# Optimization experiments

Measured on AMD Instinct MI355X. Metric: run time of the kernel, lower is better.

Reference implementation:

```python
import jax, jax.numpy as jnp
import numpy as np

B, SEG, P, H, NH = 8, 16, 256, 1024, 16
DH = H // NH
T = P + 1                 # tokens per segment (segment lord + segment_size)
L = 1 + SEG * T           # 4113
LN_EPS = 1e-12


def setup_inputs() -> dict:
    key = jax.random.key(0)
    ks = jax.random.split(key, 9)
    s = 0.02
    return {
        "hidden_states": jax.random.normal(ks[0], (B, L, H), jnp.float32),
        "Blord_w": jax.random.normal(ks[1], (H, H), jnp.float32) * s,
        "Blord_b": jnp.zeros((H,), jnp.float32),
        "seg_qw": jax.random.normal(ks[2], (SEG, H, H), jnp.float32) * s,
        "seg_kw": jax.random.normal(ks[3], (SEG, H, H), jnp.float32) * s,
        "seg_vw": jax.random.normal(ks[4], (SEG, H, H), jnp.float32) * s,
        "lord_qw": jax.random.normal(ks[5], (H, H), jnp.float32) * s,
        "lord_kw": jax.random.normal(ks[6], (H, H), jnp.float32) * s,
        "lord_vw": jax.random.normal(ks[7], (H, H), jnp.float32) * s,
        "out_w": jax.random.normal(ks[8], (H, H), jnp.float32) * s,
        "out_b": jnp.zeros((H,), jnp.float32),
        "ln_w": jnp.ones((H,), jnp.float32),
        "ln_b": jnp.zeros((H,), jnp.float32),
    }


def reference(hidden_states, Blord_w, Blord_b, seg_qw, seg_kw, seg_vw,
              lord_qw, lord_kw, lord_vw, out_w, out_b, ln_w, ln_b):
    scale = 1.0 / np.sqrt(DH).astype(np.float32)

    # global lord projection of token 0 (torch Linear: x @ W.T + b)
    Blord = hidden_states[:, 0] @ Blord_w.T + Blord_b              # [B,H]

    # per-segment local full attention (each segment has its own QKV weights)
    seg_x = hidden_states[:, 1:].reshape(B, SEG, T, H)             # [B,S,T,H]
    q = jnp.einsum('bsti,soi->bsto', seg_x, seg_qw).reshape(B, SEG, T, NH, DH)
    k = jnp.einsum('bsti,soi->bsto', seg_x, seg_kw).reshape(B, SEG, T, NH, DH)
    v = jnp.einsum('bsti,soi->bsto', seg_x, seg_vw).reshape(B, SEG, T, NH, DH)
    scores = jnp.einsum('bsqhd,bskhd->bshqk', q, k) * scale        # [B,S,NH,T,T]
    probs = jax.nn.softmax(scores, axis=-1)
    seg_out = jnp.einsum('bshqk,bskhd->bsqhd', probs, v).reshape(B, SEG, T, H)

    # global attention over lord tokens: [Blord, seg_out[:, :, 0]]
    lords_in = jnp.concatenate([Blord[:, None, :], seg_out[:, :, 0, :]], axis=1)  # [B,S+1,H]
    lq = (lords_in @ lord_qw.T).reshape(B, SEG + 1, NH, DH)
    lk = (lords_in @ lord_kw.T).reshape(B, SEG + 1, NH, DH)
    lv = (lords_in @ lord_vw.T).reshape(B, SEG + 1, NH, DH)
    lscores = jnp.einsum('bqhd,bkhd->bhqk', lq, lk) * scale        # [B,NH,S+1,S+1]
    lprobs = jax.nn.softmax(lscores, axis=-1)
    lords = jnp.einsum('bhqk,bkhd->bqhd', lprobs, lv).reshape(B, SEG + 1, H)

    # reassemble: global lord, then per segment (updated lord token, local tokens)
    seg_out = seg_out.at[:, :, 0, :].set(lords[:, 1:])
    self_outputs = jnp.concatenate(
        [lords[:, :1], seg_out.reshape(B, SEG * T, H)], axis=1)    # [B,L,H]

    # output dense + residual + LayerNorm
    h = self_outputs @ out_w.T + out_b + hidden_states
    mu = h.mean(axis=-1, keepdims=True)
    var = h.var(axis=-1, keepdims=True)
    attention_output = (h - mu) / jnp.sqrt(var + LN_EPS) * ln_w + ln_b
    return attention_output, self_outputs
```

## Files before the change

### kernel.cpp

```cpp
#include <hip/hip_runtime.h>
#include <hip/hip_bf16.h>

typedef long long ll;
typedef __attribute__((ext_vector_type(8))) short bf16x8;
typedef __attribute__((ext_vector_type(4))) float fx4;

#define B_ 8
#define SEG_ 16
#define T_ 257
#define H_ 1024
#define NH_ 16
#define L_ 4113
#define SCALE 0.125f

__device__ __forceinline__ unsigned short f2bfu(float x) {
  __hip_bfloat16 h = __float2bfloat16(x);
  return *(unsigned short*)&h;
}

__device__ __forceinline__ void gl_lds16(const void* g, void* l) {
  __builtin_amdgcn_global_load_lds((const __attribute__((address_space(1))) void*)g,
                                   (__attribute__((address_space(3))) void*)l, 16, 0, 0);
}

#define NU_HID 4211712
#define NU_W   2097152
#define NU_OW  131072
__global__ __launch_bounds__(256) void f2bf_all(
    const float* __restrict__ hid, __hip_bfloat16* __restrict__ hbf,
    const float* __restrict__ wq, const float* __restrict__ wk, const float* __restrict__ wv,
    __hip_bfloat16* __restrict__ w3,
    const float* __restrict__ ow, __hip_bfloat16* __restrict__ owb)
{
  const int NTOT = NU_HID + 3 * NU_W + NU_OW;
  for (int i = blockIdx.x * 256 + threadIdx.x; i < NTOT; i += gridDim.x * 256) {
    const float* src;
    __hip_bfloat16* dst;
    if (i < NU_HID) {
      src = hid + (ll)i * 8;
      dst = hbf + (ll)i * 8;
    } else if (i < NU_HID + 3 * NU_W) {
      int j = i - NU_HID;
      int which = j >> 21;
      int off = j & (NU_W - 1);
      const float* ws = (which == 0) ? wq : (which == 1) ? wk : wv;
      src = ws + (ll)off * 8;
      dst = w3 + (ll)j * 8;
    } else {
      int k = i - NU_HID - 3 * NU_W;
      src = ow + (ll)k * 8;
      dst = owb + (ll)k * 8;
    }
    float4 a = ((const float4*)src)[0];
    float4 b = ((const float4*)src)[1];
    union { bf16x8 v; unsigned short u[8]; } o;
    o.u[0] = f2bfu(a.x); o.u[1] = f2bfu(a.y); o.u[2] = f2bfu(a.z); o.u[3] = f2bfu(a.w);
    o.u[4] = f2bfu(b.x); o.u[5] = f2bfu(b.y); o.u[6] = f2bfu(b.z); o.u[7] = f2bfu(b.w);
    *(bf16x8*)dst = o.v;
  }
}

__global__ __launch_bounds__(256) void gemm_qkv(
    const __hip_bfloat16* __restrict__ A,
    const __hip_bfloat16* __restrict__ Wall,
    __hip_bfloat16* __restrict__ Cq,
    __hip_bfloat16* __restrict__ Ck,
    __hip_bfloat16* __restrict__ Cv)
{
  const int nwg = 24 * 17 * 16;
  const int orig = blockIdx.x + 24 * (blockIdx.y + 17 * blockIdx.z);
  const int swz = (orig & 7) * (nwg >> 3) + (orig >> 3);
  const int bx = swz % 24;
  const int t2 = swz / 24;
  const int by = t2 % 17;
  const int bz = t2 / 17;
  const int which = bx >> 3;
  const int n0 = (bx & 7) * 128;
  const int m0 = by * 128;
  const int M = B_ * T_;

  const __hip_bfloat16* W = Wall + ((ll)which * SEG_ + bz) * ((ll)H_ * H_);
  __hip_bfloat16* C = (which == 0) ? Cq : (which == 1) ? Ck : Cv;

  __shared__ __hip_bfloat16 At[2][128 * 32];
  __shared__ __hip_bfloat16 Bt[2][128 * 32];

  const int tid = threadIdx.x;
  const int lane = tid & 63;
  const int wid = tid >> 6;
  const int wm = (wid >> 1) * 64;
  const int wn = (wid & 1) * 64;

  const int r0 = tid >> 2;
  const int kc = (tid & 3) * 8;
  const int am0 = min(m0 + r0, M - 1);
  const int am1 = min(m0 + 64 + r0, M - 1);
  const ll segoff = (ll)bz * ((ll)T_ * H_);
  const ll aoff0 = (ll)(am0 / T_) * ((ll)L_ * H_) + segoff + (ll)(am0 % T_) * H_;
  const ll aoff1 = (ll)(am1 / T_) * ((ll)L_ * H_) + segoff + (ll)(am1 % T_) * H_;
  const ll boff0 = (ll)(n0 + r0) * H_;
  const ll boff1 = (ll)(n0 + 64 + r0) * H_;
  const int stA0 = r0 * 32 + kc;

  fx4 acc[4][4];
#pragma unroll
  for (int i = 0; i < 4; ++i)
#pragma unroll
    for (int j = 0; j < 4; ++j) acc[i][j] = fx4{0.f, 0.f, 0.f, 0.f};

  const int fragA = (wm + (lane & 15)) * 32 + ((lane >> 4) << 3);
  const int fragB = (wn + (lane & 15)) * 32 + ((lane >> 4) << 3);

  gl_lds16(A + aoff0 + kc, (void*)(&At[0][0] + stA0));
  gl_lds16(A + aoff1 + kc, (void*)(&At[0][0] + 2048 + stA0));
  gl_lds16(W + boff0 + kc, (void*)(&Bt[0][0] + stA0));
  gl_lds16(W + boff1 + kc, (void*)(&Bt[0][0] + 2048 + stA0));
  __syncthreads();

  int cur = 0;
  for (int k0 = 0; k0 < 1024; k0 += 32) {
    if (k0 + 32 < 1024) {
      const int kn = k0 + 32;
      const int nxt = cur ^ 1;
      gl_lds16(A + aoff0 + kn + kc, (void*)(&At[nxt][0] + stA0));
      gl_lds16(A + aoff1 + kn + kc, (void*)(&At[nxt][0] + 2048 + stA0));
      gl_lds16(W + boff0 + kn + kc, (void*)(&Bt[nxt][0] + stA0));
      gl_lds16(W + boff1 + kn + kc, (void*)(&Bt[nxt][0] + 2048 + stA0));
    }

    const __hip_bfloat16* ap = &At[cur][0] + fragA;
    const __hip_bfloat16* bp = &Bt[cur][0] + fragB;
    bf16x8 af[4], bfr[4];
#pragma unroll
    for (int f = 0; f < 4; ++f) {
      af[f]  = *(const bf16x8*)(ap + f * 16 * 32);
      bfr[f] = *(const bf16x8*)(bp + f * 16 * 32);
    }
#pragma unroll
    for (int mf = 0; mf < 4; ++mf)
#pragma unroll
      for (int nf = 0; nf < 4; ++nf)
        acc[mf][nf] = __builtin_amdgcn_mfma_f32_16x16x32_bf16(af[mf], bfr[nf], acc[mf][nf], 0, 0, 0);

    __syncthreads();
    cur ^= 1;
  }

  const int cn = n0 + wn + (lane & 15);
#pragma unroll
  for (int mf = 0; mf < 4; ++mf) {
    int mloc = m0 + wm + mf * 16 + ((lane >> 4) << 2);
#pragma unroll
    for (int r = 0; r < 4; ++r) {
      int m = mloc + r;
      if (m >= M) continue;
      ll co = ((ll)(m / T_) * SEG_ + bz) * ((ll)T_ * H_) + (ll)(m % T_) * H_;
#pragma unroll
      for (int nf = 0; nf < 4; ++nf)
        C[co + cn + nf * 16] = __float2bfloat16(acc[mf][nf][r]);
    }
  }
}

__global__ __launch_bounds__(256) void gemm_out(
    const __hip_bfloat16* __restrict__ A,
    const __hip_bfloat16* __restrict__ W,
    const float* __restrict__ bias,
    float* __restrict__ C,
    const float* __restrict__ res)
{
  const int nwg = 8 * 258;
  const int orig = blockIdx.x + 8 * blockIdx.y;
  const int swz = (orig & 7) * (nwg >> 3) + (orig >> 3);
  const int bx = swz % 8;
  const int by = swz / 8;
  const int M = B_ * L_;
  const int m0 = by * 128;
  const int n0 = bx * 128;

  __shared__ __hip_bfloat16 At[2][128 * 32];
  __shared__ __hip_bfloat16 Bt[2][128 * 32];

  const int tid = threadIdx.x;
  const int lane = tid & 63;
  const int wid = tid >> 6;
  const int wm = (wid >> 1) * 64;
  const int wn = (wid & 1) * 64;

  const int r0 = tid >> 2;
  const int kc = (tid & 3) * 8;
  const ll aoff0 = (ll)min(m0 + r0, M - 1) * H_;
  const ll aoff1 = (ll)min(m0 + 64 + r0, M - 1) * H_;
  const ll boff0 = (ll)(n0 + r0) * H_;
  const ll boff1 = (ll)(n0 + 64 + r0) * H_;
  const int stA0 = r0 * 32 + kc;

  fx4 acc[4][4];
#pragma unroll
  for (int i = 0; i < 4; ++i)
#pragma unroll
    for (int j = 0; j < 4; ++j) acc[i][j] = fx4{0.f, 0.f, 0.f, 0.f};

  const int fragA = (wm + (lane & 15)) * 32 + ((lane >> 4) << 3);
  const int fragB = (wn + (lane & 15)) * 32 + ((lane >> 4) << 3);

  gl_lds16(A + aoff0 + kc, (void*)(&At[0][0] + stA0));
  gl_lds16(A + aoff1 + kc, (void*)(&At[0][0] + 2048 + stA0));
  gl_lds16(W + boff0 + kc, (void*)(&Bt[0][0] + stA0));
  gl_lds16(W + boff1 + kc, (void*)(&Bt[0][0] + 2048 + stA0));
  __syncthreads();

  int cur = 0;
  for (int k0 = 0; k0 < 1024; k0 += 32) {
    if (k0 + 32 < 1024) {
      const int kn = k0 + 32;
      const int nxt = cur ^ 1;
      gl_lds16(A + aoff0 + kn + kc, (void*)(&At[nxt][0] + stA0));
      gl_lds16(A + aoff1 + kn + kc, (void*)(&At[nxt][0] + 2048 + stA0));
      gl_lds16(W + boff0 + kn + kc, (void*)(&Bt[nxt][0] + stA0));
      gl_lds16(W + boff1 + kn + kc, (void*)(&Bt[nxt][0] + 2048 + stA0));
    }

    const __hip_bfloat16* ap = &At[cur][0] + fragA;
    const __hip_bfloat16* bp = &Bt[cur][0] + fragB;
    bf16x8 af[4], bfr[4];
#pragma unroll
    for (int f = 0; f < 4; ++f) {
      af[f]  = *(const bf16x8*)(ap + f * 16 * 32);
      bfr[f] = *(const bf16x8*)(bp + f * 16 * 32);
    }
#pragma unroll
    for (int mf = 0; mf < 4; ++mf)
#pragma unroll
      for (int nf = 0; nf < 4; ++nf)
        acc[mf][nf] = __builtin_amdgcn_mfma_f32_16x16x32_bf16(af[mf], bfr[nf], acc[mf][nf], 0, 0, 0);

    __syncthreads();
    cur ^= 1;
  }

  const int cn = n0 + wn + (lane & 15);
#pragma unroll
  for (int mf = 0; mf < 4; ++mf) {
    int mloc = m0 + wm + mf * 16 + ((lane >> 4) << 2);
#pragma unroll
    for (int r = 0; r < 4; ++r) {
      int m = mloc + r;
      if (m >= M) continue;
#pragma unroll
      for (int nf = 0; nf < 4; ++nf) {
        int n = cn + nf * 16;
        C[(ll)m * H_ + n] = acc[mf][nf][r] + bias[n] + res[(ll)m * H_ + n];
      }
    }
  }
}

__global__ __launch_bounds__(256) void seg_attn_mfma(
    const __hip_bfloat16* __restrict__ Qb,
    const __hip_bfloat16* __restrict__ Kb,
    const __hip_bfloat16* __restrict__ Vb,
    float* __restrict__ so, __hip_bfloat16* __restrict__ sob)
{
  __shared__ __align__(16) char smem[8192 + 9216 + 4 * 4096];
  char* KsB = smem;
  char* VTB = smem + 8192;
  const int tid = threadIdx.x, lane = tid & 63, wid = tid >> 6;
  char* PB = smem + 8192 + 9216 + wid * 4096;

  const int h = blockIdx.y, bs = blockIdx.z;
  const int b = bs >> 4, s = bs & 15;
  const int q0 = blockIdx.x * 128 + wid * 32;
  const bool qvalid = (q0 <= 256);
  const ll base = (ll)bs * (T_ * H_) + h * 64;

  bf16x8 qf[2][2];
#pragma unroll
  for (int mf = 0; mf < 2; ++mf) {
    int qr = q0 + mf * 16 + (lane & 15); if (qr > 256) qr = 256;
#pragma unroll
    for (int ks = 0; ks < 2; ++ks)
      qf[mf][ks] = *(const bf16x8*)(Qb + base + (ll)qr * H_ + ks * 32 + ((lane >> 4) << 3));
  }

  float l_[2][4];
  fx4 of[2][4];
#pragma unroll
  for (int mf = 0; mf < 2; ++mf) {
#pragma unroll
    for (int r = 0; r < 4; ++r) l_[mf][r] = 0.f;
#pragma unroll
    for (int df = 0; df < 4; ++df) of[mf][df] = fx4{0.f, 0.f, 0.f, 0.f};
  }

  const int krow = tid >> 3;
  const int kc8 = tid & 7;
  const int kkp = tid & 31;
  const int vd0 = (tid >> 5) * 8;

  for (int t = 0; t < 5; ++t) {
    const int k0 = t * 64;
    __syncthreads();
    {
      int row = krow;
      int kr = k0 + row; if (kr > 256) kr = 256;
      gl_lds16(Kb + base + (ll)kr * H_ + ((kc8 ^ (row & 7)) << 3), KsB + tid * 16);
      row = krow + 32;
      kr = k0 + row; if (kr > 256) kr = 256;
      gl_lds16(Kb + base + (ll)kr * H_ + ((kc8 ^ (row & 7)) << 3), KsB + 4096 + tid * 16);
    }
    {
      int kk = kkp * 2;
      int kr0 = k0 + kk;     if (kr0 > 256) kr0 = 256;
      int kr1 = k0 + kk + 1; if (kr1 > 256) kr1 = 256;
      bf16x8 v0 = *(const bf16x8*)(Vb + base + (ll)kr0 * H_ + vd0);
      bf16x8 v1 = *(const bf16x8*)(Vb + base + (ll)kr1 * H_ + vd0);
      unsigned int* vtu = (unsigned int*)VTB;
#pragma unroll
      for (int j = 0; j < 8; ++j)
        vtu[(vd0 + j) * 36 + kkp] =
            (unsigned int)(unsigned short)v0[j] | ((unsigned int)(unsigned short)v1[j] << 16);
    }
    __syncthreads();

    if (qvalid) {
      fx4 sa[2][4];
#pragma unroll
      for (int mf = 0; mf < 2; ++mf)
#pragma unroll
        for (int nf = 0; nf < 4; ++nf) sa[mf][nf] = fx4{0.f, 0.f, 0.f, 0.f};
#pragma unroll
      for (int nf = 0; nf < 4; ++nf) {
        int key = nf * 16 + (lane & 15);
#pragma unroll
        for (int ks = 0; ks < 2; ++ks) {
          int c16 = ks * 4 + (lane >> 4);
          bf16x8 kf = *(const bf16x8*)(KsB + key * 128 + ((c16 ^ (key & 7)) << 4));
          sa[0][nf] = __builtin_amdgcn_mfma_f32_16x16x32_bf16(qf[0][ks], kf, sa[0][nf], 0, 0, 0);
          sa[1][nf] = __builtin_amdgcn_mfma_f32_16x16x32_bf16(qf[1][ks], kf, sa[1][nf], 0, 0, 0);
        }
      }
#pragma unroll
      for (int nf = 0; nf < 4; ++nf) {
        bool bad = (k0 + nf * 16 + (lane & 15)) > 256;
#pragma unroll
        for (int mf = 0; mf < 2; ++mf) {
#pragma unroll
          for (int r = 0; r < 4; ++r) {
            float p = bad ? 0.f : __expf(sa[mf][nf][r] * SCALE);
            sa[mf][nf][r] = p;
            l_[mf][r] += p;
          }
        }
      }
#pragma unroll
      for (int mf = 0; mf < 2; ++mf)
#pragma unroll
        for (int nf = 0; nf < 4; ++nf)
#pragma unroll
          for (int rp = 0; rp < 2; ++rp) {
            float v0 = sa[mf][nf][rp];
            float v2 = sa[mf][nf][rp + 2];
            float o0 = __shfl_xor(v0, 1);
            float o2 = __shfl_xor(v2, 1);
            const bool odd = (lane & 1);
            float lo = odd ? o2 : v0;
            float hi = odd ? v2 : o0;
            unsigned int pk = (unsigned int)f2bfu(lo) | ((unsigned int)f2bfu(hi) << 16);
            int row = mf * 16 + ((lane >> 4) << 2) + (odd ? rp + 2 : rp);
            int col2 = nf * 16 + (lane & 14);
            *(unsigned int*)(PB + row * 128 + ((col2 * 2) ^ ((row & 7) << 4))) = pk;
          }
#pragma unroll
      for (int kks = 0; kks < 2; ++kks) {
        bf16x8 pa[2];
#pragma unroll
        for (int mf = 0; mf < 2; ++mf) {
          int prow = mf * 16 + (lane & 15);
          int c16 = kks * 4 + (lane >> 4);
          pa[mf] = *(const bf16x8*)(PB + prow * 128 + ((c16 ^ (prow & 7)) << 4));
        }
#pragma unroll
        for (int df = 0; df < 4; ++df) {
          bf16x8 vf = *(const bf16x8*)(VTB + (df * 16 + (lane & 15)) * 144 + kks * 64 + ((lane >> 4) << 4));
          of[0][df] = __builtin_amdgcn_mfma_f32_16x16x32_bf16(pa[0], vf, of[0][df], 0, 0, 0);
          of[1][df] = __builtin_amdgcn_mfma_f32_16x16x32_bf16(pa[1], vf, of[1][df], 0, 0, 0);
        }
      }
    }
  }

  if (qvalid) {
#pragma unroll
    for (int mf = 0; mf < 2; ++mf)
#pragma unroll
      for (int r = 0; r < 4; ++r) {
        float rs = l_[mf][r];
        rs += __shfl_xor(rs, 1);
        rs += __shfl_xor(rs, 2);
        rs += __shfl_xor(rs, 4);
        rs += __shfl_xor(rs, 8);
        l_[mf][r] = rs;
      }
#pragma unroll
    for (int mf = 0; mf < 2; ++mf)
#pragma unroll
      for (int r = 0; r < 4; ++r) {
        int q = q0 + mf * 16 + ((lane >> 4) << 2) + r;
        if (q > 256) continue;
        float inv = 1.f / l_[mf][r];
        ll rowoff = ((ll)b * L_ + 1 + (ll)s * T_ + q) * H_ + h * 64;
#pragma unroll
        for (int df = 0; df < 4; ++df) {
          int d = df * 16 + (lane & 15);
          float v = of[mf][df][r] * inv;
          so[rowoff + d] = v;
          sob[rowoff + d] = __float2bfloat16(v);
        }
      }
  }
}

__global__ __launch_bounds__(256) void gemm_bt(
    const float* __restrict__ X, ll xbs,
    const float* __restrict__ W,
    const float* __restrict__ bias,
    float* __restrict__ C, ll cbs,
    int M, int K)
{
  const int tid = threadIdx.x;
  const int n0 = blockIdx.x * 64;

  __shared__ float Xt[16][68];
  __shared__ float Wt[16][68];

  const int lr = tid >> 2;
  const int lc = (tid & 3) << 2;
  const int mload = min(lr, M - 1);
  const ll xoff = (ll)mload * xbs;
  const ll woff = (ll)(n0 + lr) * K;

  const int tr = tid >> 4;
  const int tc = tid & 15;

  float acc[4][4];
#pragma unroll
  for (int i = 0; i < 4; ++i)
#pragma unroll
    for (int j = 0; j < 4; ++j) acc[i][j] = 0.f;

  for (int k0 = 0; k0 < K; k0 += 16) {
    float4 xv = *(const float4*)(X + xoff + k0 + lc);
    float4 wv = *(const float4*)(W + woff + k0 + lc);
    __syncthreads();
    Xt[lc + 0][lr] = xv.x; Xt[lc + 1][lr] = xv.y; Xt[lc + 2][lr] = xv.z; Xt[lc + 3][lr] = xv.w;
    Wt[lc + 0][lr] = wv.x; Wt[lc + 1][lr] = wv.y; Wt[lc + 2][lr] = wv.z; Wt[lc + 3][lr] = wv.w;
    __syncthreads();
#pragma unroll
    for (int kk = 0; kk < 16; ++kk) {
      float4 xa = *(const float4*)&Xt[kk][tr << 2];
      float4 wb = *(const float4*)&Wt[kk][tc << 2];
      float xa_[4] = {xa.x, xa.y, xa.z, xa.w};
      float wb_[4] = {wb.x, wb.y, wb.z, wb.w};
#pragma unroll
      for (int i = 0; i < 4; ++i)
#pragma unroll
        for (int j = 0; j < 4; ++j)
          acc[i][j] = fmaf(xa_[i], wb_[j], acc[i][j]);
    }
  }

#pragma unroll
  for (int i = 0; i < 4; ++i) {
    int m = (tr << 2) + i;
    if (m >= M) continue;
#pragma unroll
    for (int j = 0; j < 4; ++j) {
      int n = n0 + (tc << 2) + j;
      C[(ll)m * cbs + n] = acc[i][j] + (bias ? bias[n] : 0.f);
    }
  }
}

__global__ __launch_bounds__(256) void lord_proj(
    const float* __restrict__ X,
    const float* __restrict__ Wq, const float* __restrict__ Wk, const float* __restrict__ Wv,
    float* __restrict__ Cq, float* __restrict__ Ck, float* __restrict__ Cv)
{
  const float* W = (blockIdx.z == 0) ? Wq : (blockIdx.z == 1) ? Wk : Wv;
  float* C = (blockIdx.z == 0) ? Cq : (blockIdx.z == 1) ? Ck : Cv;
  const int M = 136, K = 1024;

  const int tid = threadIdx.x;
  const int m0 = blockIdx.y * 64;
  const int n0 = blockIdx.x * 64;

  __shared__ float Xt[16][68];
  __shared__ float Wt[16][68];

  const int lr = tid >> 2;
  const int lc = (tid & 3) << 2;
  const int mload = min(m0 + lr, M - 1);
  const ll xoff = (ll)mload * K;
  const ll woff = (ll)(n0 + lr) * K;

  const int tr = tid >> 4;
  const int tc = tid & 15;

  float acc[4][4];
#pragma unroll
  for (int i = 0; i < 4; ++i)
#pragma unroll
    for (int j = 0; j < 4; ++j) acc[i][j] = 0.f;

  for (int k0 = 0; k0 < K; k0 += 16) {
    float4 xv = *(const float4*)(X + xoff + k0 + lc);
    float4 wv = *(const float4*)(W + woff + k0 + lc);
    __syncthreads();
    Xt[lc + 0][lr] = xv.x; Xt[lc + 1][lr] = xv.y; Xt[lc + 2][lr] = xv.z; Xt[lc + 3][lr] = xv.w;
    Wt[lc + 0][lr] = wv.x; Wt[lc + 1][lr] = wv.y; Wt[lc + 2][lr] = wv.z; Wt[lc + 3][lr] = wv.w;
    __syncthreads();
#pragma unroll
    for (int kk = 0; kk < 16; ++kk) {
      float4 xa = *(const float4*)&Xt[kk][tr << 2];
      float4 wb = *(const float4*)&Wt[kk][tc << 2];
      float xa_[4] = {xa.x, xa.y, xa.z, xa.w};
      float wb_[4] = {wb.x, wb.y, wb.z, wb.w};
#pragma unroll
      for (int i = 0; i < 4; ++i)
#pragma unroll
        for (int j = 0; j < 4; ++j)
          acc[i][j] = fmaf(xa_[i], wb_[j], acc[i][j]);
    }
  }

#pragma unroll
  for (int i = 0; i < 4; ++i) {
    int m = m0 + (tr << 2) + i;
    if (m >= M) continue;
#pragma unroll
    for (int j = 0; j < 4; ++j)
      C[(ll)m * 1024 + n0 + (tc << 2) + j] = acc[i][j];
  }
}

__global__ __launch_bounds__(256) void copy_lords_in(
    const float* __restrict__ so, float* __restrict__ lin)
{
  int b = blockIdx.x / SEG_, s = blockIdx.x % SEG_;
  int i = threadIdx.x * 4;
  *(float4*)(lin + ((ll)(b * 17 + 1 + s)) * H_ + i) =
      *(const float4*)(so + ((ll)b * L_ + 1 + (ll)s * T_) * H_ + i);
}

__global__ __launch_bounds__(256) void lord_attn2(
    const float* __restrict__ lq, const float* __restrict__ lk,
    const float* __restrict__ lv, float* __restrict__ so,
    __hip_bfloat16* __restrict__ sob)
{
  const int b = blockIdx.x, h = blockIdx.y;
  const int tid = threadIdx.x, lane = tid & 63, wid = tid >> 6;
  __shared__ float Qs[17][64], Ks[17][64], Vs[17][64];
  for (int t = tid; t < 17 * 64; t += 256) {
    int r = t >> 6, c = t & 63;
    ll g = ((ll)(b * 17 + r)) * H_ + h * 64 + c;
    Qs[r][c] = lq[g];
    Ks[r][c] = lk[g];
    Vs[r][c] = lv[g];
  }
  __syncthreads();
  for (int q = wid; q < 17; q += 4) {
    float qd = Qs[q][lane];
    float sc[17];
#pragma unroll
    for (int k = 0; k < 17; ++k) {
      float p = qd * Ks[k][lane];
      p += __shfl_xor(p, 1);  p += __shfl_xor(p, 2);  p += __shfl_xor(p, 4);
      p += __shfl_xor(p, 8);  p += __shfl_xor(p, 16); p += __shfl_xor(p, 32);
      sc[k] = p * SCALE;
    }
    float mx = sc[0];
#pragma unroll
    for (int k = 1; k < 17; ++k) mx = fmaxf(mx, sc[k]);
    float l = 0.f;
#pragma unroll
    for (int k = 0; k < 17; ++k) { sc[k] = __expf(sc[k] - mx); l += sc[k]; }
    float invl = 1.f / l;
    float o = 0.f;
#pragma unroll
    for (int k = 0; k < 17; ++k) o = fmaf(sc[k], Vs[k][lane], o);
    o *= invl;
    ll row = (q == 0) ? (ll)b * L_ : ((ll)b * L_ + 1 + (ll)(q - 1) * T_);
    so[row * H_ + h * 64 + lane] = o;
    sob[row * H_ + h * 64 + lane] = __float2bfloat16(o);
  }
}

__global__ __launch_bounds__(256) void ln_inplace(
    float* __restrict__ hbuf, const float* __restrict__ w, const float* __restrict__ bgain)
{
  const ll row = blockIdx.x;
  const int tid = threadIdx.x;
  float4 x = *(float4*)(hbuf + row * H_ + tid * 4);
  float s = x.x + x.y + x.z + x.w;
  float s2 = x.x * x.x + x.y * x.y + x.z * x.z + x.w * x.w;
#pragma unroll
  for (int off = 32; off >= 1; off >>= 1) {
    s  += __shfl_down(s, off, 64);
    s2 += __shfl_down(s2, off, 64);
  }
  __shared__ float red[2][4];
  int wid = tid >> 6;
  if ((tid & 63) == 0) { red[0][wid] = s; red[1][wid] = s2; }
  __syncthreads();
  s  = red[0][0] + red[0][1] + red[0][2] + red[0][3];
  s2 = red[1][0] + red[1][1] + red[1][2] + red[1][3];
  const float mean = s * (1.f / H_);
  float var = s2 * (1.f / H_) - mean * mean;
  var = fmaxf(var, 0.f);
  const float inv = rsqrtf(var + 1e-12f);
  float4 g = *(const float4*)(w + tid * 4);
  float4 bb = *(const float4*)(bgain + tid * 4);
  float4 y;
  y.x = (x.x - mean) * inv * g.x + bb.x;
  y.y = (x.y - mean) * inv * g.y + bb.y;
  y.z = (x.z - mean) * inv * g.z + bb.z;
  y.w = (x.w - mean) * inv * g.w + bb.w;
  *(float4*)(hbuf + row * H_ + tid * 4) = y;
}

extern "C" void kernel_launch(void* const* d_in, const int* in_sizes, int n_in,
                              void* d_out, int out_size, void* d_ws, size_t ws_size,
                              hipStream_t stream)
{
  const float* hidden  = (const float*)d_in[0];
  const float* Blord_w = (const float*)d_in[1];
  const float* Blord_b = (const float*)d_in[2];
  const float* seg_qw  = (const float*)d_in[3];
  const float* seg_kw  = (const float*)d_in[4];
  const float* seg_vw  = (const float*)d_in[5];
  const float* lord_qw = (const float*)d_in[6];
  const float* lord_kw = (const float*)d_in[7];
  const float* lord_vw = (const float*)d_in[8];
  const float* out_w   = (const float*)d_in[9];
  const float* out_b   = (const float*)d_in[10];
  const float* ln_w    = (const float*)d_in[11];
  const float* ln_b    = (const float*)d_in[12];

  float* attn_out = (float*)d_out;
  float* self_out = (float*)d_out + (ll)B_ * L_ * H_;

  const ll QKV = (ll)B_ * SEG_ * T_ * H_;
  const ll SHH = (ll)SEG_ * H_ * H_;
  __hip_bfloat16* qb = (__hip_bfloat16*)attn_out;
  __hip_bfloat16* kb = qb + QKV;
  __hip_bfloat16* hbf = (__hip_bfloat16*)self_out;
  __hip_bfloat16* vb = (__hip_bfloat16*)d_ws;
  __hip_bfloat16* wslot3 = vb + QKV;
  __hip_bfloat16* sob = wslot3;
  __hip_bfloat16* outw_bf = wslot3 + 3 * SHH;
  float* lords_in = (float*)(outw_bf + (ll)H_ * H_);
  float* lqw_ = lords_in + 136 * 1024;
  float* lkw_ = lqw_ + 136 * 1024;
  float* lvw_ = lkw_ + 136 * 1024;

  dim3 blk(256);

  f2bf_all<<<dim3(2048), blk, 0, stream>>>(
      hidden, hbf, seg_qw, seg_kw, seg_vw, wslot3, out_w, outw_bf);

  gemm_qkv<<<dim3(24, 17, 16), blk, 0, stream>>>(hbf + H_, wslot3, qb, kb, vb);

  gemm_bt<<<dim3(16), blk, 0, stream>>>(
      hidden, (ll)L_ * H_, Blord_w, Blord_b, lords_in, (ll)17 * H_, B_, H_);

  seg_attn_mfma<<<dim3(3, NH_, B_ * SEG_), blk, 0, stream>>>(qb, kb, vb, self_out, sob);

  copy_lords_in<<<dim3(B_ * SEG_), blk, 0, stream>>>(self_out, lords_in);

  lord_proj<<<dim3(16, 3, 3), blk, 0, stream>>>(
      lords_in, lord_qw, lord_kw, lord_vw, lqw_, lkw_, lvw_);

  lord_attn2<<<dim3(B_, NH_), blk, 0, stream>>>(lqw_, lkw_, lvw_, self_out, sob);

  gemm_out<<<dim3(8, 258), blk, 0, stream>>>(sob, outw_bf, out_b, attn_out, hidden);

  ln_inplace<<<dim3(B_ * L_), blk, 0, stream>>>(attn_out, ln_w, ln_b);
}
```

Measured before the change: 876.0 us.

## Triple-buffer GEMM K-loop with vmcnt waits and XOR-swizzled LDS tiles

Both the per-segment QKV GEMM and the output GEMM move from a double-buffered LDS pipeline to a three-stage one, prefetching two K-tiles ahead. They use explicit s_waitcnt vmcnt counts with raw barriers instead of __syncthreads. The global source column is XOR-swizzled per row, and the fragment read offset applies the matching swizzle, to cut LDS bank conflicts on the MFMA operand loads. This raises LDS use per block by half and relies on hand-counted outstanding loads being correct.

```diff
diff --git a/kernel.cpp b/kernel.cpp
--- a/kernel.cpp
+++ b/kernel.cpp
@@ -82,8 +82,8 @@
   const __hip_bfloat16* W = Wall + ((ll)which * SEG_ + bz) * ((ll)H_ * H_);
   __hip_bfloat16* C = (which == 0) ? Cq : (which == 1) ? Ck : Cv;
 
-  __shared__ __hip_bfloat16 At[2][128 * 32];
-  __shared__ __hip_bfloat16 Bt[2][128 * 32];
+  __shared__ __hip_bfloat16 At[3][128 * 32];
+  __shared__ __hip_bfloat16 Bt[3][128 * 32];
 
   const int tid = threadIdx.x;
   const int lane = tid & 63;
@@ -92,7 +92,9 @@
   const int wn = (wid & 1) * 64;
 
   const int r0 = tid >> 2;
-  const int kc = (tid & 3) * 8;
+  const int p = tid & 3;
+  const int kc  = p * 8;
+  const int kcs = (p ^ ((r0 >> 1) & 3)) * 8;
   const int am0 = min(m0 + r0, M - 1);
   const int am1 = min(m0 + 64 + r0, M - 1);
   const ll segoff = (ll)bz * ((ll)T_ * H_);
@@ -108,28 +110,31 @@
 #pragma unroll
     for (int j = 0; j < 4; ++j) acc[i][j] = fx4{0.f, 0.f, 0.f, 0.f};
 
-  const int fragA = (wm + (lane & 15)) * 32 + ((lane >> 4) << 3);
-  const int fragB = (wn + (lane & 15)) * 32 + ((lane >> 4) << 3);
-
-  gl_lds16(A + aoff0 + kc, (void*)(&At[0][0] + stA0));
-  gl_lds16(A + aoff1 + kc, (void*)(&At[0][0] + 2048 + stA0));
-  gl_lds16(W + boff0 + kc, (void*)(&Bt[0][0] + stA0));
-  gl_lds16(W + boff1 + kc, (void*)(&Bt[0][0] + 2048 + stA0));
-  __syncthreads();
-
-  int cur = 0;
-  for (int k0 = 0; k0 < 1024; k0 += 32) {
-    if (k0 + 32 < 1024) {
-      const int kn = k0 + 32;
-      const int nxt = cur ^ 1;
-      gl_lds16(A + aoff0 + kn + kc, (void*)(&At[nxt][0] + stA0));
-      gl_lds16(A + aoff1 + kn + kc, (void*)(&At[nxt][0] + 2048 + stA0));
-      gl_lds16(W + boff0 + kn + kc, (void*)(&Bt[nxt][0] + stA0));
-      gl_lds16(W + boff1 + kn + kc, (void*)(&Bt[nxt][0] + 2048 + stA0));
-    }
-
-    const __hip_bfloat16* ap = &At[cur][0] + fragA;
-    const __hip_bfloat16* bp = &Bt[cur][0] + fragB;
+  const int sw = ((lane & 15) >> 1) & 3;
+  const int fragA = (wm + (lane & 15)) * 32 + (((lane >> 4) ^ sw) << 3);
+  const int fragB = (wn + (lane & 15)) * 32 + (((lane >> 4) ^ sw) << 3);
+
+#define STAGE_QKV(buf, kt) do { const int kk = (kt) * 32; \
+    gl_lds16(A + aoff0 + kk + kcs, (void*)(&At[buf][0] + stA0)); \
+    gl_lds16(A + aoff1 + kk + kcs, (void*)(&At[buf][0] + 2048 + stA0)); \
+    gl_lds16(W + boff0 + kk + kcs, (void*)(&Bt[buf][0] + stA0)); \
+    gl_lds16(W + boff1 + kk + kcs, (void*)(&Bt[buf][0] + 2048 + stA0)); } while (0)
+
+  STAGE_QKV(0, 0);
+  STAGE_QKV(1, 1);
+  for (int t = 0; t < 32; ++t) {
+    __builtin_amdgcn_s_barrier();
+    asm volatile("" ::: "memory");
+    if (t + 2 < 32) { const int b3 = (t + 2) % 3; STAGE_QKV(b3, t + 2); }
+    if (t < 30)       asm volatile("s_waitcnt vmcnt(8)" ::: "memory");
+    else if (t == 30) asm volatile("s_waitcnt vmcnt(4)" ::: "memory");
+    else              asm volatile("s_waitcnt vmcnt(0)" ::: "memory");
+    __builtin_amdgcn_s_barrier();
+    asm volatile("" ::: "memory");
+
+    const int cb = t % 3;
+    const __hip_bfloat16* ap = &At[cb][0] + fragA;
+    const __hip_bfloat16* bp = &Bt[cb][0] + fragB;
     bf16x8 af[4], bfr[4];
 #pragma unroll
     for (int f = 0; f < 4; ++f) {
@@ -141,10 +146,8 @@
 #pragma unroll
       for (int nf = 0; nf < 4; ++nf)
         acc[mf][nf] = __builtin_amdgcn_mfma_f32_16x16x32_bf16(af[mf], bfr[nf], acc[mf][nf], 0, 0, 0);
-
-    __syncthreads();
-    cur ^= 1;
-  }
+  }
+#undef STAGE_QKV
 
   const int cn = n0 + wn + (lane & 15);
 #pragma unroll
@@ -178,8 +181,8 @@
   const int m0 = by * 128;
   const int n0 = bx * 128;
 
-  __shared__ __hip_bfloat16 At[2][128 * 32];
-  __shared__ __hip_bfloat16 Bt[2][128 * 32];
+  __shared__ __hip_bfloat16 At[3][128 * 32];
+  __shared__ __hip_bfloat16 Bt[3][128 * 32];
 
   const int tid = threadIdx.x;
   const int lane = tid & 63;
@@ -188,7 +191,9 @@
   const int wn = (wid & 1) * 64;
 
   const int r0 = tid >> 2;
-  const int kc = (tid & 3) * 8;
+  const int p = tid & 3;
+  const int kc  = p * 8;
+  const int kcs = (p ^ ((r0 >> 1) & 3)) * 8;
   const ll aoff0 = (ll)min(m0 + r0, M - 1) * H_;
   const ll aoff1 = (ll)min(m0 + 64 + r0, M - 1) * H_;
   const ll boff0 = (ll)(n0 + r0) * H_;
@@ -201,28 +206,31 @@
 #pragma unroll
     for (int j = 0; j < 4; ++j) acc[i][j] = fx4{0.f, 0.f, 0.f, 0.f};
 
-  const int fragA = (wm + (lane & 15)) * 32 + ((lane >> 4) << 3);
-  const int fragB = (wn + (lane & 15)) * 32 + ((lane >> 4) << 3);
-
-  gl_lds16(A + aoff0 + kc, (void*)(&At[0][0] + stA0));
-  gl_lds16(A + aoff1 + kc, (void*)(&At[0][0] + 2048 + stA0));
-  gl_lds16(W + boff0 + kc, (void*)(&Bt[0][0] + stA0));
-  gl_lds16(W + boff1 + kc, (void*)(&Bt[0][0] + 2048 + stA0));
-  __syncthreads();
-
-  int cur = 0;
-  for (int k0 = 0; k0 < 1024; k0 += 32) {
-    if (k0 + 32 < 1024) {
-      const int kn = k0 + 32;
-      const int nxt = cur ^ 1;
-      gl_lds16(A + aoff0 + kn + kc, (void*)(&At[nxt][0] + stA0));
-      gl_lds16(A + aoff1 + kn + kc, (void*)(&At[nxt][0] + 2048 + stA0));
-      gl_lds16(W + boff0 + kn + kc, (void*)(&Bt[nxt][0] + stA0));
-      gl_lds16(W + boff1 + kn + kc, (void*)(&Bt[nxt][0] + 2048 + stA0));
-    }
-
-    const __hip_bfloat16* ap = &At[cur][0] + fragA;
-    const __hip_bfloat16* bp = &Bt[cur][0] + fragB;
+  const int sw = ((lane & 15) >> 1) & 3;
+  const int fragA = (wm + (lane & 15)) * 32 + (((lane >> 4) ^ sw) << 3);
+  const int fragB = (wn + (lane & 15)) * 32 + (((lane >> 4) ^ sw) << 3);
+
+#define STAGE_O(buf, kt) do { const int kk = (kt) * 32; \
+    gl_lds16(A + aoff0 + kk + kcs, (void*)(&At[buf][0] + stA0)); \
+    gl_lds16(A + aoff1 + kk + kcs, (void*)(&At[buf][0] + 2048 + stA0)); \
+    gl_lds16(W + boff0 + kk + kcs, (void*)(&Bt[buf][0] + stA0)); \
+    gl_lds16(W + boff1 + kk + kcs, (void*)(&Bt[buf][0] + 2048 + stA0)); } while (0)
+
+  STAGE_O(0, 0);
+  STAGE_O(1, 1);
+  for (int t = 0; t < 32; ++t) {
+    __builtin_amdgcn_s_barrier();
+    asm volatile("" ::: "memory");
+    if (t + 2 < 32) { const int b3 = (t + 2) % 3; STAGE_O(b3, t + 2); }
+    if (t < 30)       asm volatile("s_waitcnt vmcnt(8)" ::: "memory");
+    else if (t == 30) asm volatile("s_waitcnt vmcnt(4)" ::: "memory");
+    else              asm volatile("s_waitcnt vmcnt(0)" ::: "memory");
+    __builtin_amdgcn_s_barrier();
+    asm volatile("" ::: "memory");
+
+    const int cb = t % 3;
+    const __hip_bfloat16* ap = &At[cb][0] + fragA;
+    const __hip_bfloat16* bp = &Bt[cb][0] + fragB;
     bf16x8 af[4], bfr[4];
 #pragma unroll
     for (int f = 0; f < 4; ++f) {
@@ -234,10 +242,8 @@
 #pragma unroll
       for (int nf = 0; nf < 4; ++nf)
         acc[mf][nf] = __builtin_amdgcn_mfma_f32_16x16x32_bf16(af[mf], bfr[nf], acc[mf][nf], 0, 0, 0);
-
-    __syncthreads();
-    cur ^= 1;
-  }
+  }
+#undef STAGE_O
 
   const int cn = n0 + wn + (lane & 15);
 #pragma unroll
@@ -347,9 +353,9 @@
         for (int mf = 0; mf < 2; ++mf) {
 #pragma unroll
           for (int r = 0; r < 4; ++r) {
-            float p = bad ? 0.f : __expf(sa[mf][nf][r] * SCALE);
-            sa[mf][nf][r] = p;
-            l_[mf][r] += p;
+            float pexp = bad ? 0.f : __expf(sa[mf][nf][r] * SCALE);
+            sa[mf][nf][r] = pexp;
+            l_[mf][r] += pexp;
           }
         }
       }
```

Result: faster. 851.1 us (-2.8%).
